# Kernel tuning notes

Measured on AMD Instinct MI355X. Metric: run time of the kernel, lower is better.

Reference implementation:

```python
import jax, jax.numpy as jnp
import numpy as np

N, D, NBINS, NUM_IDS = 8192, 256, 64, 512
MAX_DIST = 2.0  # initial +/- histogram range from __init__ (max_dist default)
EPS_DIST = 1e-12
EPS_HIST = 1e-6


def setup_inputs() -> dict:
    key = jax.random.key(0)
    kx, kt = jax.random.split(key)
    x = jax.random.normal(kx, (N, D), dtype=jnp.float32)
    targets = jax.random.randint(kt, (N,), 0, NUM_IDS, dtype=jnp.int64)
    histogram = jnp.ones((NBINS,), dtype=jnp.float32)  # buffer initial state
    return {"x": x, "targets": targets, "histogram": histogram}


def reference(x, targets, histogram):
    n = x.shape[0]
    nbins = histogram.shape[0]
    # pairwise euclidean distances: [n, n]
    sq = jnp.sum(x * x, axis=1)
    dist = jnp.sqrt(jnp.clip(sq[:, None] + sq[None, :] - 2.0 * (x @ x.T), EPS_DIST, None))
    mask = targets[:, None] == targets[None, :]
    neg_inf = jnp.array(-jnp.inf, dtype=dist.dtype)
    pos_inf = jnp.array(jnp.inf, dtype=dist.dtype)
    pos_dist = jnp.max(jnp.where(mask, dist, neg_inf), axis=1)  # hardest positive per row
    neg_dist = jnp.min(jnp.where(mask, pos_inf, dist), axis=1)  # hardest negative per row
    hist_val = pos_dist - neg_dist
    # _compute_histogram: widen range by batch extremes (torch uses .item() on detached values)
    hv = jax.lax.stop_gradient(hist_val)
    max_val = jnp.maximum(jnp.max(hv), MAX_DIST)
    min_val = jnp.minimum(jnp.min(hv), -MAX_DIST)
    bin_width = (max_val - min_val) / (nbins - 1)
    lo = jnp.floor((hv - min_val) / bin_width).astype(jnp.int32)
    hi = jnp.clip(lo + 1, 0, nbins - 1)
    alpha = 1.0 - (hv - min_val - lo.astype(hv.dtype) * bin_width) / bin_width
    hist = jnp.zeros((nbins,), dtype=hv.dtype).at[lo].add(alpha).at[hi].add(1.0 - alpha)
    hist = hist / (jnp.sum(hist) + EPS_HIST)
    # first call: _stats_initialized is False -> momentum = 1.0, new buffer = hist
    new_histogram = hist
    pdf = new_histogram / jnp.sum(new_histogram)
    cdf = jnp.cumsum(pdf)
    bin_idx = jnp.floor((hv - min_val) / bin_width).astype(jnp.int32)
    weight = cdf[bin_idx]  # detached weighting (built entirely from stop_gradient values)
    loss = -jnp.mean(neg_dist * weight) + jnp.mean(pos_dist * weight)
    return loss
```

## Files before the change

kernel.cpp:

```cpp
#include <hip/hip_runtime.h>
#include <math.h>

#define Nn 8192
#define Dd 256
#define NBINS 64
#define NSPLIT 8

typedef __attribute__((ext_vector_type(8))) short short8;
typedef __attribute__((ext_vector_type(4))) float f32x4;

#define GLOAD16(g, l)                                                        \
  __builtin_amdgcn_global_load_lds(                                          \
      (const __attribute__((address_space(1))) void*)(g),                    \
      (__attribute__((address_space(3))) void*)(l), 16, 0, 0)

static __device__ __forceinline__ unsigned short f2bf(float f) {
  unsigned int u = __float_as_uint(f);
  u = (u + 0x7fffu + ((u >> 16) & 1u)) >> 16;
  return (unsigned short)u;
}
static __device__ __forceinline__ unsigned int enc_ord(float f) {
  unsigned int u = __float_as_uint(f);
  return (u & 0x80000000u) ? ~u : (u | 0x80000000u);
}
static __device__ __forceinline__ float dec_ord(unsigned int u) {
  unsigned int b2 = (u & 0x80000000u) ? (u ^ 0x80000000u) : ~u;
  return __uint_as_float(b2);
}

__global__ __launch_bounds__(256) void prep_kernel(const float* __restrict__ x,
                                                   const int* __restrict__ lab,
                                                   unsigned short* __restrict__ xb,
                                                   float2* __restrict__ sqlab,
                                                   unsigned int* __restrict__ pos2,
                                                   unsigned int* __restrict__ neg2,
                                                   unsigned int* __restrict__ gmm,
                                                   float* __restrict__ ghist,
                                                   float* __restrict__ ghsum) {
  const int w = threadIdx.x >> 6;
  const int lane = threadIdx.x & 63;
  const int row = blockIdx.x * 4 + w;
  const float4 v = *(const float4*)(x + (size_t)row * Dd + lane * 4);
  ushort4 b;
  b.x = f2bf(v.x); b.y = f2bf(v.y); b.z = f2bf(v.z); b.w = f2bf(v.w);
  *(ushort4*)(xb + (size_t)row * Dd + lane * 4) = b;
  float s = v.x * v.x + v.y * v.y + v.z * v.z + v.w * v.w;
#pragma unroll
  for (int off = 32; off >= 1; off >>= 1) s += __shfl_xor(s, off);
  if (lane == 0) {
    sqlab[row] = make_float2(s, __int_as_float(lab[row]));
    pos2[row] = 0x007fffffu;
    neg2[row] = 0xff800000u;
  }
  if (blockIdx.x == 0 && threadIdx.x < NBINS) {
    ghist[threadIdx.x] = 0.0f;
    ghsum[threadIdx.x] = 0.0f;
    if (threadIdx.x == 0) { gmm[0] = 0x007fffffu; gmm[1] = 0xff800000u; }
  }
}

static __device__ __forceinline__ void stage_a(const unsigned short* __restrict__ xb,
                                               int r0, int hh, unsigned short* buf, int t) {
#pragma unroll
  for (int i = 0; i < 8; ++i) {
    const int c = i * 256 + t;
    const int col = c >> 4;
    const int kq = (c & 15) ^ (col & 15);
    GLOAD16(xb + (size_t)(r0 + col) * Dd + hh * 128 + kq * 8, buf + (size_t)c * 8);
  }
}
static __device__ __forceinline__ void stage_b(const unsigned short* __restrict__ xb,
                                               int c0, int hh, unsigned short* buf, int t) {
#pragma unroll
  for (int i = 0; i < 4; ++i) {
    const int c = i * 256 + t;
    const int col = c >> 4;
    const int kq = (c & 15) ^ (col & 15);
    GLOAD16(xb + (size_t)(c0 + col) * Dd + hh * 128 + kq * 8, buf + (size_t)c * 8);
  }
}

__global__ __launch_bounds__(256, 2) void pairwise_kernel(const unsigned short* __restrict__ xb,
                                                          const float2* __restrict__ sqlab,
                                                          unsigned int* __restrict__ pos2,
                                                          unsigned int* __restrict__ neg2) {
  __shared__ __align__(16) unsigned short Us[4096 * 8];
  __shared__ __align__(16) float2 sl_s[1024];
  __shared__ int lab_s[128];

  const int t = threadIdx.x;
  const int lane = t & 63;
  const int w = t >> 6;
  const int wr = w >> 1;
  const int wc = w & 1;
  const int c_l = lane & 15;
  const int kq_l = lane >> 4;
  const int rows0 = blockIdx.x * 128;
  const int cbase = blockIdx.y * (Nn / NSPLIT);

  stage_a(xb, rows0, 0, Us, t);
  stage_a(xb, rows0, 1, Us + 2048 * 8, t);
#pragma unroll
  for (int i = 0; i < 4; ++i) sl_s[i * 256 + t] = sqlab[cbase + i * 256 + t];
  if (t < 128) lab_s[t] = __float_as_int(sqlab[rows0 + t].y);
  __syncthreads();

  const short8* Uv = (const short8*)Us;
  short8 af[32];
#pragma unroll
  for (int k2 = 0; k2 < 8; ++k2)
#pragma unroll
    for (int m = 0; m < 4; ++m) {
      const int kqf = k2 * 4 + kq_l;
      const int rl = wr * 64 + m * 16 + c_l;
      af[k2 * 4 + m] = Uv[(kqf >> 4) * 2048 + rl * 16 + ((kqf & 15) ^ (rl & 15))];
    }
  int labp[8];
#pragma unroll
  for (int m = 0; m < 4; ++m)
#pragma unroll
    for (int pp = 0; pp < 2; ++pp) {
      const int r0 = wr * 64 + m * 16 + kq_l * 4 + 2 * pp;
      labp[m * 2 + pp] = (lab_s[r0] & 0xffff) | (lab_s[r0 + 1] << 16);
    }
  __syncthreads();

  unsigned short* const Bs0 = Us;
  unsigned short* const Bs1 = Us + 2048 * 8;

  stage_b(xb, cbase, 0, Bs0, t);
  stage_b(xb, cbase, 1, Bs0 + 1024 * 8, t);

  const int cc0 = wc * 32 + c_l;
  const int cc1 = wc * 32 + 16 + c_l;
  float pmax[16], nmin[16];
#pragma unroll
  for (int i = 0; i < 16; ++i) { pmax[i] = -INFINITY; nmin[i] = INFINITY; }

  int cur = 0;
#pragma unroll 1
  for (int ct = 0; ct < 16; ++ct) {
    unsigned short* const bufR = cur ? Bs1 : Bs0;
    unsigned short* const bufW = cur ? Bs0 : Bs1;

    __syncthreads();
    if (ct < 15) {
      stage_b(xb, cbase + (ct + 1) * 64, 0, bufW, t);
      stage_b(xb, cbase + (ct + 1) * 64, 1, bufW + 1024 * 8, t);
    }

    f32x4 acc[4][2];
#pragma unroll
    for (int m = 0; m < 4; ++m)
#pragma unroll
      for (int n = 0; n < 2; ++n) acc[m][n] = (f32x4){0.f, 0.f, 0.f, 0.f};

    {
      const short8* Bv = (const short8*)bufR;
#pragma unroll
      for (int ks = 0; ks < 4; ++ks) {
        const short8 bf0 = Bv[cc0 * 16 + ((ks * 4 + kq_l) ^ (cc0 & 15))];
        const short8 bf1 = Bv[cc1 * 16 + ((ks * 4 + kq_l) ^ (cc1 & 15))];
#pragma unroll
        for (int m = 0; m < 4; ++m) {
          acc[m][0] = __builtin_amdgcn_mfma_f32_16x16x32_bf16(af[ks * 4 + m], bf0, acc[m][0], 0, 0, 0);
          acc[m][1] = __builtin_amdgcn_mfma_f32_16x16x32_bf16(af[ks * 4 + m], bf1, acc[m][1], 0, 0, 0);
        }
      }
    }
    {
      const short8* Bv = (const short8*)(bufR + 1024 * 8);
#pragma unroll
      for (int ks = 0; ks < 4; ++ks) {
        const short8 bf0 = Bv[cc0 * 16 + ((ks * 4 + kq_l) ^ (cc0 & 15))];
        const short8 bf1 = Bv[cc1 * 16 + ((ks * 4 + kq_l) ^ (cc1 & 15))];
#pragma unroll
        for (int m = 0; m < 4; ++m) {
          acc[m][0] = __builtin_amdgcn_mfma_f32_16x16x32_bf16(af[(4 + ks) * 4 + m], bf0, acc[m][0], 0, 0, 0);
          acc[m][1] = __builtin_amdgcn_mfma_f32_16x16x32_bf16(af[(4 + ks) * 4 + m], bf1, acc[m][1], 0, 0, 0);
        }
      }
    }

    {
      const float2 sl0 = sl_s[ct * 64 + cc0];
      const float2 sl1 = sl_s[ct * 64 + cc1];
#pragma unroll
      for (int n = 0; n < 2; ++n) {
        const float sc = (n == 0) ? sl0.x : sl1.x;
        const int lc = __float_as_int((n == 0) ? sl0.y : sl1.y);
#pragma unroll
        for (int idx = 0; idx < 16; ++idx) {
          const int m = idx >> 2, q = idx & 3;
          const float g = fmaf(-2.0f, acc[m][n][q], sc);
          const int lr = (labp[idx >> 1] >> ((idx & 1) * 16)) & 0xffff;
          const bool same = (lr == lc);
          pmax[idx] = same ? fmaxf(pmax[idx], g) : pmax[idx];
          nmin[idx] = same ? nmin[idx] : fminf(nmin[idx], g);
        }
      }
    }
    cur ^= 1;
  }

#pragma unroll
  for (int i = 0; i < 16; ++i) {
    float p = pmax[i], nn2 = nmin[i];
#pragma unroll
    for (int off = 1; off < 16; off <<= 1) {
      p = fmaxf(p, __shfl_xor(p, off));
      nn2 = fminf(nn2, __shfl_xor(nn2, off));
    }
    if (c_l == 0) {
      const int rowg = rows0 + wr * 64 + (i >> 2) * 16 + kq_l * 4 + (i & 3);
      atomicMax(&pos2[rowg], enc_ord(p));
      atomicMin(&neg2[rowg], enc_ord(nn2));
    }
  }
}

__global__ __launch_bounds__(512) void finalize_a_kernel(const float2* __restrict__ sqlab,
                                                         const unsigned int* __restrict__ pos2,
                                                         const unsigned int* __restrict__ neg2,
                                                         float* __restrict__ hv_g,
                                                         unsigned int* __restrict__ gmm) {
  const int i = blockIdx.x * 512 + threadIdx.x;
  const int lane = threadIdx.x & 63;
  const float s = sqlab[i].x;
  const float p2 = fmaxf(s + dec_ord(pos2[i]), 1e-12f);
  const float n2 = fmaxf(s + dec_ord(neg2[i]), 1e-12f);
  const float hv = sqrtf(p2) - sqrtf(n2);
  hv_g[i] = hv;
  float lmax = hv, lmin = hv;
#pragma unroll
  for (int off = 32; off >= 1; off >>= 1) {
    lmax = fmaxf(lmax, __shfl_xor(lmax, off));
    lmin = fminf(lmin, __shfl_xor(lmin, off));
  }
  if (lane == 0) {
    atomicMax(&gmm[0], enc_ord(lmax));
    atomicMin(&gmm[1], enc_ord(lmin));
  }
}

__global__ __launch_bounds__(512) void finalize_b_kernel(const float* __restrict__ hv_g,
                                                         const unsigned int* __restrict__ gmm,
                                                         float* __restrict__ ghist,
                                                         float* __restrict__ ghsum) {
  __shared__ float hist_s[NBINS];
  __shared__ float hsum_s[NBINS];
  const int t = threadIdx.x;
  if (t < NBINS) { hist_s[t] = 0.0f; hsum_s[t] = 0.0f; }
  const float maxv = fmaxf(dec_ord(gmm[0]), 2.0f);
  const float minv = fminf(dec_ord(gmm[1]), -2.0f);
  const float bw = (maxv - minv) / (float)(NBINS - 1);
  __syncthreads();

  const int i = blockIdx.x * 512 + t;
  const float hv = hv_g[i];
  int lo = (int)floorf((hv - minv) / bw);
  lo = min(max(lo, 0), NBINS - 1);
  const int hi = min(lo + 1, NBINS - 1);
  const float alpha = 1.0f - (hv - minv - (float)lo * bw) / bw;
  atomicAdd(&hist_s[lo], alpha);
  atomicAdd(&hist_s[hi], 1.0f - alpha);
  atomicAdd(&hsum_s[lo], hv);
  __syncthreads();

  if (t < NBINS) {
    atomicAdd(&ghist[t], hist_s[t]);
    atomicAdd(&ghsum[t], hsum_s[t]);
  }
}

__global__ __launch_bounds__(64) void finalize_c_kernel(const float* __restrict__ ghist,
                                                        const float* __restrict__ ghsum,
                                                        float* __restrict__ out) {
  const int t = threadIdx.x;
  const float h = ghist[t];
  float total = h;
#pragma unroll
  for (int off = 32; off >= 1; off >>= 1) total += __shfl_xor(total, off);
  const float hn = h / (total + 1e-6f);
  float s2 = hn;
#pragma unroll
  for (int off = 32; off >= 1; off >>= 1) s2 += __shfl_xor(s2, off);
  const float pdf = hn / s2;
  float c = pdf;
#pragma unroll
  for (int off = 1; off < 64; off <<= 1) {
    const float u = __shfl_up(c, off);
    if (t >= off) c += u;
  }
  float acc = c * ghsum[t];
#pragma unroll
  for (int off = 32; off >= 1; off >>= 1) acc += __shfl_xor(acc, off);
  if (t == 0) out[0] = acc / (float)Nn;
}

extern "C" void kernel_launch(void* const* d_in, const int* in_sizes, int n_in,
                              void* d_out, int out_size, void* d_ws, size_t ws_size,
                              hipStream_t stream) {
  const float* x = (const float*)d_in[0];
  const int* targets = (const int*)d_in[1];
  float* out = (float*)d_out;

  char* p = (char*)d_ws;
  unsigned short* xb = (unsigned short*)p;  p += (size_t)Nn * Dd * 2;
  float2* sqlab = (float2*)p;               p += (size_t)Nn * 8;
  unsigned int* pos2 = (unsigned int*)p;    p += (size_t)Nn * 4;
  unsigned int* neg2 = (unsigned int*)p;    p += (size_t)Nn * 4;
  float* hv_g = (float*)p;                  p += (size_t)Nn * 4;
  unsigned int* gmm = (unsigned int*)p;     p += 64;
  float* ghist = (float*)p;                 p += NBINS * 4;
  float* ghsum = (float*)p;

  prep_kernel<<<Nn / 4, 256, 0, stream>>>(x, targets, xb, sqlab, pos2, neg2, gmm, ghist, ghsum);
  pairwise_kernel<<<dim3(Nn / 128, NSPLIT), 256, 0, stream>>>(xb, sqlab, pos2, neg2);
  finalize_a_kernel<<<Nn / 512, 512, 0, stream>>>(sqlab, pos2, neg2, hv_g, gmm);
  finalize_b_kernel<<<Nn / 512, 512, 0, stream>>>(hv_g, gmm, ghist, ghsum);
  finalize_c_kernel<<<1, 64, 0, stream>>>(ghist, ghsum, out);
}
```

Before: 63.01 us.

## Fold final reduction into histogram kernel and software-pipeline LDS B-fragment loads

Removes the separate single-block finalize_c launch: finalize_b now counts finished blocks with an atomic counter, and the last block computes the CDF-weighted loss. The pairwise inner loop moves into a do_tile helper unrolled twice. That removes the runtime buffer select, and each B fragment is loaded from LDS one k-step ahead of its MFMAs so the reads overlap the math. The epilogue also interleaves the two column halves. The changes save one kernel launch and some LDS latency, at the cost of extra registers for the prefetched fragments and a last-block atomic handshake.

```diff
diff --git a/kernel.cpp b/kernel.cpp
--- a/kernel.cpp
+++ b/kernel.cpp
@@ -36,7 +36,8 @@
                                                    unsigned int* __restrict__ neg2,
                                                    unsigned int* __restrict__ gmm,
                                                    float* __restrict__ ghist,
-                                                   float* __restrict__ ghsum) {
+                                                   float* __restrict__ ghsum,
+                                                   unsigned int* __restrict__ cnt) {
   const int w = threadIdx.x >> 6;
   const int lane = threadIdx.x & 63;
   const int row = blockIdx.x * 4 + w;
@@ -55,7 +56,7 @@
   if (blockIdx.x == 0 && threadIdx.x < NBINS) {
     ghist[threadIdx.x] = 0.0f;
     ghsum[threadIdx.x] = 0.0f;
-    if (threadIdx.x == 0) { gmm[0] = 0x007fffffu; gmm[1] = 0xff800000u; }
+    if (threadIdx.x == 0) { gmm[0] = 0x007fffffu; gmm[1] = 0xff800000u; cnt[0] = 0u; }
   }
 }
 
@@ -77,6 +78,64 @@
     const int col = c >> 4;
     const int kq = (c & 15) ^ (col & 15);
     GLOAD16(xb + (size_t)(c0 + col) * Dd + hh * 128 + kq * 8, buf + (size_t)c * 8);
+  }
+}
+
+static __device__ __forceinline__ void do_tile(
+    const unsigned short* __restrict__ bufR, unsigned short* __restrict__ bufW,
+    int ct, int cbase, const unsigned short* __restrict__ xb,
+    const short8 (&af)[32], const int (&labp)[8], const float2* __restrict__ sl_s,
+    float (&pmax)[16], float (&nmin)[16], int t, int cc0, int cc1, int kq_l) {
+  __syncthreads();
+  if (ct < 15) {
+    stage_b(xb, cbase + (ct + 1) * 64, 0, bufW, t);
+    stage_b(xb, cbase + (ct + 1) * 64, 1, bufW + 1024 * 8, t);
+  }
+
+  f32x4 acc[4][2];
+#pragma unroll
+  for (int m = 0; m < 4; ++m)
+#pragma unroll
+    for (int n = 0; n < 2; ++n) acc[m][n] = (f32x4){0.f, 0.f, 0.f, 0.f};
+
+  const short8* const Bv0 = (const short8*)bufR;
+  const short8* const Bv1 = (const short8*)(bufR + 1024 * 8);
+  const int x0 = cc0 & 15, x1 = cc1 & 15;
+
+  short8 b0 = Bv0[cc0 * 16 + (kq_l ^ x0)];
+  short8 b1 = Bv0[cc1 * 16 + (kq_l ^ x1)];
+#pragma unroll
+  for (int ks = 0; ks < 8; ++ks) {
+    short8 n0, n1;
+    if (ks < 7) {
+      const short8* const B = (ks + 1 < 4) ? Bv0 : Bv1;
+      const int o = ((ks + 1) & 3) * 4 + kq_l;
+      n0 = B[cc0 * 16 + (o ^ x0)];
+      n1 = B[cc1 * 16 + (o ^ x1)];
+    }
+#pragma unroll
+    for (int m = 0; m < 4; ++m) {
+      acc[m][0] = __builtin_amdgcn_mfma_f32_16x16x32_bf16(af[ks * 4 + m], b0, acc[m][0], 0, 0, 0);
+      acc[m][1] = __builtin_amdgcn_mfma_f32_16x16x32_bf16(af[ks * 4 + m], b1, acc[m][1], 0, 0, 0);
+    }
+    if (ks < 7) { b0 = n0; b1 = n1; }
+  }
+
+  const float2 sl0 = sl_s[ct * 64 + cc0];
+  const float2 sl1 = sl_s[ct * 64 + cc1];
+  const int lc0 = __float_as_int(sl0.y);
+  const int lc1 = __float_as_int(sl1.y);
+#pragma unroll
+  for (int idx = 0; idx < 16; ++idx) {
+    const int m = idx >> 2, q = idx & 3;
+    const int lr = (labp[idx >> 1] >> ((idx & 1) * 16)) & 0xffff;
+    const float g0 = fmaf(-2.0f, acc[m][0][q], sl0.x);
+    const float g1 = fmaf(-2.0f, acc[m][1][q], sl1.x);
+    const bool s0 = (lr == lc0), s1 = (lr == lc1);
+    pmax[idx] = s0 ? fmaxf(pmax[idx], g0) : pmax[idx];
+    nmin[idx] = s0 ? nmin[idx] : fminf(nmin[idx], g0);
+    pmax[idx] = s1 ? fmaxf(pmax[idx], g1) : pmax[idx];
+    nmin[idx] = s1 ? nmin[idx] : fminf(nmin[idx], g1);
   }
 }
 
@@ -137,70 +196,10 @@
 #pragma unroll
   for (int i = 0; i < 16; ++i) { pmax[i] = -INFINITY; nmin[i] = INFINITY; }
 
-  int cur = 0;
 #pragma unroll 1
-  for (int ct = 0; ct < 16; ++ct) {
-    unsigned short* const bufR = cur ? Bs1 : Bs0;
-    unsigned short* const bufW = cur ? Bs0 : Bs1;
-
-    __syncthreads();
-    if (ct < 15) {
-      stage_b(xb, cbase + (ct + 1) * 64, 0, bufW, t);
-      stage_b(xb, cbase + (ct + 1) * 64, 1, bufW + 1024 * 8, t);
-    }
-
-    f32x4 acc[4][2];
-#pragma unroll
-    for (int m = 0; m < 4; ++m)
-#pragma unroll
-      for (int n = 0; n < 2; ++n) acc[m][n] = (f32x4){0.f, 0.f, 0.f, 0.f};
-
-    {
-      const short8* Bv = (const short8*)bufR;
-#pragma unroll
-      for (int ks = 0; ks < 4; ++ks) {
-        const short8 bf0 = Bv[cc0 * 16 + ((ks * 4 + kq_l) ^ (cc0 & 15))];
-        const short8 bf1 = Bv[cc1 * 16 + ((ks * 4 + kq_l) ^ (cc1 & 15))];
-#pragma unroll
-        for (int m = 0; m < 4; ++m) {
-          acc[m][0] = __builtin_amdgcn_mfma_f32_16x16x32_bf16(af[ks * 4 + m], bf0, acc[m][0], 0, 0, 0);
-          acc[m][1] = __builtin_amdgcn_mfma_f32_16x16x32_bf16(af[ks * 4 + m], bf1, acc[m][1], 0, 0, 0);
-        }
-      }
-    }
-    {
-      const short8* Bv = (const short8*)(bufR + 1024 * 8);
-#pragma unroll
-      for (int ks = 0; ks < 4; ++ks) {
-        const short8 bf0 = Bv[cc0 * 16 + ((ks * 4 + kq_l) ^ (cc0 & 15))];
-        const short8 bf1 = Bv[cc1 * 16 + ((ks * 4 + kq_l) ^ (cc1 & 15))];
-#pragma unroll
-        for (int m = 0; m < 4; ++m) {
-          acc[m][0] = __builtin_amdgcn_mfma_f32_16x16x32_bf16(af[(4 + ks) * 4 + m], bf0, acc[m][0], 0, 0, 0);
-          acc[m][1] = __builtin_amdgcn_mfma_f32_16x16x32_bf16(af[(4 + ks) * 4 + m], bf1, acc[m][1], 0, 0, 0);
-        }
-      }
-    }
-
-    {
-      const float2 sl0 = sl_s[ct * 64 + cc0];
-      const float2 sl1 = sl_s[ct * 64 + cc1];
-#pragma unroll
-      for (int n = 0; n < 2; ++n) {
-        const float sc = (n == 0) ? sl0.x : sl1.x;
-        const int lc = __float_as_int((n == 0) ? sl0.y : sl1.y);
-#pragma unroll
-        for (int idx = 0; idx < 16; ++idx) {
-          const int m = idx >> 2, q = idx & 3;
-          const float g = fmaf(-2.0f, acc[m][n][q], sc);
-          const int lr = (labp[idx >> 1] >> ((idx & 1) * 16)) & 0xffff;
-          const bool same = (lr == lc);
-          pmax[idx] = same ? fmaxf(pmax[idx], g) : pmax[idx];
-          nmin[idx] = same ? nmin[idx] : fminf(nmin[idx], g);
-        }
-      }
-    }
-    cur ^= 1;
+  for (int ct2 = 0; ct2 < 8; ++ct2) {
+    do_tile(Bs0, Bs1, 2 * ct2,     cbase, xb, af, labp, sl_s, pmax, nmin, t, cc0, cc1, kq_l);
+    do_tile(Bs1, Bs0, 2 * ct2 + 1, cbase, xb, af, labp, sl_s, pmax, nmin, t, cc0, cc1, kq_l);
   }
 
 #pragma unroll
@@ -246,9 +245,12 @@
 __global__ __launch_bounds__(512) void finalize_b_kernel(const float* __restrict__ hv_g,
                                                          const unsigned int* __restrict__ gmm,
                                                          float* __restrict__ ghist,
-                                                         float* __restrict__ ghsum) {
+                                                         float* __restrict__ ghsum,
+                                                         unsigned int* __restrict__ cnt,
+                                                         float* __restrict__ out) {
   __shared__ float hist_s[NBINS];
   __shared__ float hsum_s[NBINS];
+  __shared__ unsigned int s_last;
   const int t = threadIdx.x;
   if (t < NBINS) { hist_s[t] = 0.0f; hsum_s[t] = 0.0f; }
   const float maxv = fmaxf(dec_ord(gmm[0]), 2.0f);
@@ -271,31 +273,33 @@
     atomicAdd(&ghist[t], hist_s[t]);
     atomicAdd(&ghsum[t], hsum_s[t]);
   }
-}
-
-__global__ __launch_bounds__(64) void finalize_c_kernel(const float* __restrict__ ghist,
-                                                        const float* __restrict__ ghsum,
-                                                        float* __restrict__ out) {
-  const int t = threadIdx.x;
-  const float h = ghist[t];
-  float total = h;
-#pragma unroll
-  for (int off = 32; off >= 1; off >>= 1) total += __shfl_xor(total, off);
-  const float hn = h / (total + 1e-6f);
-  float s2 = hn;
-#pragma unroll
-  for (int off = 32; off >= 1; off >>= 1) s2 += __shfl_xor(s2, off);
-  const float pdf = hn / s2;
-  float c = pdf;
-#pragma unroll
-  for (int off = 1; off < 64; off <<= 1) {
-    const float u = __shfl_up(c, off);
-    if (t >= off) c += u;
-  }
-  float acc = c * ghsum[t];
-#pragma unroll
-  for (int off = 32; off >= 1; off >>= 1) acc += __shfl_xor(acc, off);
-  if (t == 0) out[0] = acc / (float)Nn;
+  __threadfence();
+  if (t == 0) s_last = atomicAdd(cnt, 1u);
+  __syncthreads();
+  if (s_last != (unsigned int)(gridDim.x - 1)) return;
+
+  if (t < NBINS) {
+    const float h = __hip_atomic_load(&ghist[t], __ATOMIC_RELAXED, __HIP_MEMORY_SCOPE_AGENT);
+    const float hs = __hip_atomic_load(&ghsum[t], __ATOMIC_RELAXED, __HIP_MEMORY_SCOPE_AGENT);
+    float total = h;
+#pragma unroll
+    for (int off = 32; off >= 1; off >>= 1) total += __shfl_xor(total, off);
+    const float hn = h / (total + 1e-6f);
+    float s2 = hn;
+#pragma unroll
+    for (int off = 32; off >= 1; off >>= 1) s2 += __shfl_xor(s2, off);
+    const float pdf = hn / s2;
+    float c = pdf;
+#pragma unroll
+    for (int off = 1; off < 64; off <<= 1) {
+      const float u = __shfl_up(c, off);
+      if (t >= off) c += u;
+    }
+    float acc = c * hs;
+#pragma unroll
+    for (int off = 32; off >= 1; off >>= 1) acc += __shfl_xor(acc, off);
+    if (t == 0) out[0] = acc / (float)Nn;
+  }
 }
 
 extern "C" void kernel_launch(void* const* d_in, const int* in_sizes, int n_in,
@@ -313,11 +317,11 @@
   float* hv_g = (float*)p;                  p += (size_t)Nn * 4;
   unsigned int* gmm = (unsigned int*)p;     p += 64;
   float* ghist = (float*)p;                 p += NBINS * 4;
-  float* ghsum = (float*)p;
-
-  prep_kernel<<<Nn / 4, 256, 0, stream>>>(x, targets, xb, sqlab, pos2, neg2, gmm, ghist, ghsum);
+  float* ghsum = (float*)p;                 p += NBINS * 4;
+  unsigned int* cnt = (unsigned int*)p;
+
+  prep_kernel<<<Nn / 4, 256, 0, stream>>>(x, targets, xb, sqlab, pos2, neg2, gmm, ghist, ghsum, cnt);
   pairwise_kernel<<<dim3(Nn / 128, NSPLIT), 256, 0, stream>>>(xb, sqlab, pos2, neg2);
   finalize_a_kernel<<<Nn / 512, 512, 0, stream>>>(sqlab, pos2, neg2, hv_g, gmm);
-  finalize_b_kernel<<<Nn / 512, 512, 0, stream>>>(hv_g, gmm, ghist, ghsum);
-  finalize_c_kernel<<<1, 64, 0, stream>>>(ghist, ghsum, out);
-}
+  finalize_b_kernel<<<Nn / 512, 512, 0, stream>>>(hv_g, gmm, ghist, ghsum, cnt, out);
+}
```

Result: slower. 71.91 us (+14.1%).
